# Kernel tuning notes

Measured on AMD Instinct MI355X. Metric: run time of the kernel, lower is better.

## Reference

```python
import jax, jax.numpy as jnp
import numpy as np

N = 50000
NEG_SLOPE = 0.2


def add_self_loops(edge_index, n):
    loop = jnp.arange(n, dtype=edge_index.dtype)
    return jnp.concatenate([edge_index, jnp.stack([loop, loop])], axis=1)


def gatv2_conv(x, edge_index, Wl, bl, Wr, br, att, bias):
    """PyG GATv2Conv (share_weights=False, concat=True, add_self_loops applied by caller).
    x: [N, Fin]; edge_index: [2, E] with row0=src(j), row1=dst(i); att: [H, D].
    Returns (out [N, H*D], alpha [E, H])."""
    src, dst = edge_index[0], edge_index[1]
    H, D = att.shape
    n = x.shape[0]
    xl = (x @ Wl + bl).reshape(n, H, D)   # source-side transform
    xr = (x @ Wr + br).reshape(n, H, D)   # target-side transform
    e = jax.nn.leaky_relu(xl[src] + xr[dst], NEG_SLOPE)        # [E, H, D]
    logit = jnp.einsum('ehd,hd->eh', e, att)                    # [E, H]
    # segment softmax over edges grouped by target node
    lmax = jax.ops.segment_max(logit, dst, num_segments=n)      # [N, H]
    ex = jnp.exp(logit - lmax[dst])
    denom = jax.ops.segment_sum(ex, dst, num_segments=n)
    alpha = ex / denom[dst]                                     # [E, H]
    out = jax.ops.segment_sum(alpha[:, :, None] * xl[src], dst, num_segments=n)  # [N, H, D]
    return out.reshape(n, H * D) + bias, alpha


def setup_inputs() -> dict:
    key = jax.random.key(0)
    ks = jax.random.split(key, 16)
    E = 400000
    x = jax.random.normal(ks[0], (N, 23), dtype=jnp.float32)
    edge_index = jax.random.randint(ks[1], (2, E), 0, N, dtype=jnp.int64)
    H1, D1 = 8, 64
    F1 = H1 * D1  # 512
    s = 0.1
    return {
        'x': x,
        'edge_index': edge_index,
        'Wl1': jax.random.normal(ks[2], (23, F1), dtype=jnp.float32) * s,
        'bl1': jnp.zeros((F1,), jnp.float32),
        'Wr1': jax.random.normal(ks[3], (23, F1), dtype=jnp.float32) * s,
        'br1': jnp.zeros((F1,), jnp.float32),
        'att1': jax.random.normal(ks[4], (H1, D1), dtype=jnp.float32) * s,
        'bias1': jnp.zeros((F1,), jnp.float32),
        'Wl2': jax.random.normal(ks[5], (F1, 1), dtype=jnp.float32) * s,
        'bl2': jnp.zeros((1,), jnp.float32),
        'Wr2': jax.random.normal(ks[6], (F1, 1), dtype=jnp.float32) * s,
        'br2': jnp.zeros((1,), jnp.float32),
        'att2': jax.random.normal(ks[7], (1, 1), dtype=jnp.float32) * s,
        'bias2': jnp.zeros((1,), jnp.float32),
    }


def reference(x, edge_index, Wl1, bl1, Wr1, br1, att1, bias1,
              Wl2, bl2, Wr2, br2, att2, bias2):
    ei = add_self_loops(edge_index, N)
    h, _ = gatv2_conv(x, ei, Wl1, bl1, Wr1, br1, att1, bias1)
    h = jax.nn.relu(h)
    h, alpha = gatv2_conv(h, ei, Wl2, bl2, Wr2, br2, att2, bias2)
    return h, alpha
```

## Files before the change

kernel.cpp:

```cpp
#include <hip/hip_runtime.h>
#include <hip/hip_cooperative_groups.h>
#include <math.h>

namespace cg = cooperative_groups;

#define NN 50000
#define E0 400000
#define EE 450000
#define FF 512
#define G1 2048
#define NPB 25
#define MAXD 64
#define LOG2E 1.44269504f
#define NCU 256

typedef _Float16 h2 __attribute__((ext_vector_type(2)));

__device__ __forceinline__ h2 uas_h2(unsigned u) { union { unsigned u; h2 h; } c; c.u = u; return c.h; }
__device__ __forceinline__ unsigned h2as_u(h2 h) { union { unsigned u; h2 h; } c; c.h = h; return c.u; }
__device__ __forceinline__ unsigned packh(float a, float b) {
    h2 hh = { (_Float16)a, (_Float16)b };
    return h2as_u(hh);
}
__device__ __forceinline__ float leaky(float v) { return fmaxf(v, 0.2f * v); }

template <int CTRL>
__device__ __forceinline__ float dpp_add(float v) {
    int x = __builtin_bit_cast(int, v);
    int y = __builtin_amdgcn_update_dpp(0, x, CTRL, 0xF, 0xF, true);
    return v + __builtin_bit_cast(float, y);
}


__device__ __forceinline__ void phase_scatter(
    int e0, int stride, const int* __restrict__ ei,
    int* __restrict__ cnt, int* __restrict__ src_sl)
{
    for (int e = e0; e < EE; e += stride) {
        int src, dst;
        if (e < E0) { src = ei[e]; dst = ei[E0 + e]; }
        else        { src = e - E0; dst = src; }
        int p = atomicAdd(&cnt[dst], 1);
        if (p < MAXD) src_sl[(size_t)dst * MAXD + p] = src;
    }
}

__device__ __forceinline__ void phase_layer1(
    int l, int wid, int wstep,
    const uint4* __restrict__ xlh, const uint4* __restrict__ xrh,
    const float* __restrict__ att, const float* __restrict__ bias1,
    const float* __restrict__ Wl2, const float* __restrict__ bl2,
    const float* __restrict__ Wr2, const float* __restrict__ br2,
    const int* __restrict__ cnt, const int* __restrict__ src_sl,
    float* __restrict__ xl2, float* __restrict__ xr2)
{
    float4 atA = ((const float4*)att)[2 * l];
    float4 atB = ((const float4*)att)[2 * l + 1];
    h2 a6_0 = { (_Float16)(0.6f * LOG2E * atA.x), (_Float16)(0.6f * LOG2E * atA.y) };
    h2 a6_1 = { (_Float16)(0.6f * LOG2E * atA.z), (_Float16)(0.6f * LOG2E * atA.w) };
    h2 a6_2 = { (_Float16)(0.6f * LOG2E * atB.x), (_Float16)(0.6f * LOG2E * atB.y) };
    h2 a6_3 = { (_Float16)(0.6f * LOG2E * atB.z), (_Float16)(0.6f * LOG2E * atB.w) };
    h2 a4_0 = { (_Float16)(0.4f * LOG2E * atA.x), (_Float16)(0.4f * LOG2E * atA.y) };
    h2 a4_1 = { (_Float16)(0.4f * LOG2E * atA.z), (_Float16)(0.4f * LOG2E * atA.w) };
    h2 a4_2 = { (_Float16)(0.4f * LOG2E * atB.x), (_Float16)(0.4f * LOG2E * atB.y) };
    h2 a4_3 = { (_Float16)(0.4f * LOG2E * atB.z), (_Float16)(0.4f * LOG2E * atB.w) };
    float bl2v = bl2[0], br2v = br2[0];

    int i = wid;
    int dg0 = 0, myj = 0; uint4 xq = {0, 0, 0, 0};
    if (i < NN) {
        dg0 = cnt[i];
        myj = src_sl[(size_t)i * MAXD + l];
        xq  = xrh[(size_t)i * 64 + l];
    }

    for (; i < NN; i += wstep) {
        int dg = dg0; if (dg > MAXD) dg = MAXD;

        int s0 = 0;
        int s1 = (dg > 1) ? 1 : 0;
        int s2 = (dg > 2) ? 2 : s1;
        int s3 = (dg > 3) ? 3 : s2;
        uint4 ra = xlh[(size_t)__builtin_amdgcn_readlane(myj, s0) * 64 + l];
        uint4 rb = xlh[(size_t)__builtin_amdgcn_readlane(myj, s1) * 64 + l];
        uint4 rc = xlh[(size_t)__builtin_amdgcn_readlane(myj, s2) * 64 + l];
        uint4 rd = xlh[(size_t)__builtin_amdgcn_readlane(myj, s3) * 64 + l];

        int inext = i + wstep;
        int dg_n = 0, myj_n = 0; uint4 xq_n = {0, 0, 0, 0};
        if (inext < NN) {
            dg_n  = cnt[inext];
            myj_n = src_sl[(size_t)inext * MAXD + l];
            xq_n  = xrh[(size_t)inext * 64 + l];
        }

        h2 q0 = uas_h2(xq.x), q1 = uas_h2(xq.y), q2 = uas_h2(xq.z), q3 = uas_h2(xq.w);

        float s = 0.f;
        h2 A0 = { 0, 0 }, A1 = { 0, 0 }, A2 = { 0, 0 }, A3 = { 0, 0 };

#define PROC(RV)                                                               \
        {                                                                      \
            h2 p0 = uas_h2(RV.x), p1 = uas_h2(RV.y),                           \
               p2 = uas_h2(RV.z), p3 = uas_h2(RV.w);                           \
            h2 t0 = p0 + q0, t1 = p1 + q1, t2 = p2 + q2, t3 = p3 + q3;         \
            h2 b0 = uas_h2(h2as_u(t0) & 0x7fff7fffu);                          \
            h2 b1 = uas_h2(h2as_u(t1) & 0x7fff7fffu);                          \
            h2 b2 = uas_h2(h2as_u(t2) & 0x7fff7fffu);                          \
            h2 b3 = uas_h2(h2as_u(t3) & 0x7fff7fffu);                          \
            float part = 0.f;                                                  \
            part = __builtin_amdgcn_fdot2(a6_0, t0, part, false);              \
            part = __builtin_amdgcn_fdot2(a4_0, b0, part, false);              \
            part = __builtin_amdgcn_fdot2(a6_1, t1, part, false);              \
            part = __builtin_amdgcn_fdot2(a4_1, b1, part, false);              \
            part = __builtin_amdgcn_fdot2(a6_2, t2, part, false);              \
            part = __builtin_amdgcn_fdot2(a4_2, b2, part, false);              \
            part = __builtin_amdgcn_fdot2(a6_3, t3, part, false);              \
            part = __builtin_amdgcn_fdot2(a4_3, b3, part, false);              \
            part = dpp_add<0xB1>(part);                                        \
            part = dpp_add<0x4E>(part);                                        \
            part = dpp_add<0x141>(part);                                       \
            float wv = exp2f(part);                                            \
            s += wv;                                                           \
            _Float16 wh = (_Float16)wv;                                        \
            h2 w2 = { wh, wh };                                                \
            A0 += w2 * p0;                                                     \
            A1 += w2 * p1;                                                     \
            A2 += w2 * p2;                                                     \
            A3 += w2 * p3;                                                     \
        }

        int p = 0;
        for (;;) {
            PROC(ra);
            if (++p >= dg) break;
            { int sl = p + 3 < dg ? p + 3 : dg - 1;
              ra = xlh[(size_t)__builtin_amdgcn_readlane(myj, sl) * 64 + l]; }
            PROC(rb);
            if (++p >= dg) break;
            { int sl = p + 3 < dg ? p + 3 : dg - 1;
              rb = xlh[(size_t)__builtin_amdgcn_readlane(myj, sl) * 64 + l]; }
            PROC(rc);
            if (++p >= dg) break;
            { int sl = p + 3 < dg ? p + 3 : dg - 1;
              rc = xlh[(size_t)__builtin_amdgcn_readlane(myj, sl) * 64 + l]; }
            PROC(rd);
            if (++p >= dg) break;
            { int sl = p + 3 < dg ? p + 3 : dg - 1;
              rd = xlh[(size_t)__builtin_amdgcn_readlane(myj, sl) * 64 + l]; }
        }
#undef PROC

        float inv = 1.f / s;
        float4 bA = ((const float4*)bias1)[2 * l];
        float4 bB = ((const float4*)bias1)[2 * l + 1];
        float h0 = fmaxf(fmaf((float)A0[0], inv, bA.x), 0.f);
        float h1 = fmaxf(fmaf((float)A0[1], inv, bA.y), 0.f);
        float h2v = fmaxf(fmaf((float)A1[0], inv, bA.z), 0.f);
        float h3 = fmaxf(fmaf((float)A1[1], inv, bA.w), 0.f);
        float h4 = fmaxf(fmaf((float)A2[0], inv, bB.x), 0.f);
        float h5 = fmaxf(fmaf((float)A2[1], inv, bB.y), 0.f);
        float h6 = fmaxf(fmaf((float)A3[0], inv, bB.z), 0.f);
        float h7 = fmaxf(fmaf((float)A3[1], inv, bB.w), 0.f);

        float4 wlA = ((const float4*)Wl2)[2 * l];
        float4 wlB = ((const float4*)Wl2)[2 * l + 1];
        float4 wrA = ((const float4*)Wr2)[2 * l];
        float4 wrB = ((const float4*)Wr2)[2 * l + 1];
        float pl = h0 * wlA.x + h1 * wlA.y + h2v * wlA.z + h3 * wlA.w
                 + h4 * wlB.x + h5 * wlB.y + h6 * wlB.z + h7 * wlB.w;
        float pr = h0 * wrA.x + h1 * wrA.y + h2v * wrA.z + h3 * wrA.w
                 + h4 * wrB.x + h5 * wrB.y + h6 * wrB.z + h7 * wrB.w;
#pragma unroll
        for (int o = 32; o > 0; o >>= 1) {
            pl += __shfl_xor(pl, o, 64);
            pr += __shfl_xor(pr, o, 64);
        }
        if (l == 0) {
            xl2[i] = pl + bl2v;
            xr2[i] = pr + br2v;
        }

        dg0 = dg_n; myj = myj_n; xq = xq_n;
    }
}

__device__ __forceinline__ void phase_l2a(
    int i0, int stride,
    const float* __restrict__ xl2, const float* __restrict__ xr2,
    const float* __restrict__ att2, const float* __restrict__ bias2,
    const int* __restrict__ cnt, const int* __restrict__ src_sl,
    float* __restrict__ out, float* __restrict__ invs)
{
    for (int i = i0; i < NN; i += stride) {
        int dg = cnt[i]; if (dg > MAXD) dg = MAXD;
        const int* sp = src_sl + (size_t)i * MAXD;
        float xri = xr2[i];
        float a2l = att2[0] * LOG2E;
        float s = 0.f, num = 0.f;
        float va = xl2[sp[0]];
        float vb = (1 < dg) ? xl2[sp[1]] : 0.f;
        float vc = (2 < dg) ? xl2[sp[2]] : 0.f;
        float vd = (3 < dg) ? xl2[sp[3]] : 0.f;
        for (int p = 0; p < dg; p++) {
            float v = va; va = vb; vb = vc; vc = vd;
            vd = (p + 4 < dg) ? xl2[sp[p + 4]] : 0.f;
            float w = exp2f(leaky(v + xri) * a2l);
            s += w;
            num = fmaf(w, v, num);
        }
        out[i] = num / s + bias2[0];
        invs[i] = 1.f / s;
    }
}

__device__ __forceinline__ void phase_l2b(
    int e0, int stride,
    const float* __restrict__ xl2, const float* __restrict__ xr2,
    const float* __restrict__ att2, const int* __restrict__ ei,
    const float* __restrict__ invs, float* __restrict__ out)
{
    for (int e = e0; e < EE; e += stride) {
        int src, dst;
        if (e < E0) { src = ei[e]; dst = ei[E0 + e]; }
        else        { src = e - E0; dst = src; }
        float a2l = att2[0] * LOG2E;
        float lg = leaky(xl2[src] + xr2[dst]) * a2l;
        out[NN + e] = exp2f(lg) * invs[dst];
    }
}


__global__ __launch_bounds__(256) void k_pregemm(
    const float* __restrict__ x,
    const float* __restrict__ Wl1, const float* __restrict__ bl1,
    const float* __restrict__ Wr1, const float* __restrict__ br1,
    unsigned* __restrict__ xlh, unsigned* __restrict__ xrh,
    int* __restrict__ cnt)
{
    __shared__ unsigned sxh[NPB * 12];
    int b = blockIdx.x, t = threadIdx.x;

    int z = b * 256 + t;
    if (z < NN) cnt[z] = 0;

    int i0 = b * NPB;
    int i1 = i0 + NPB; if (i1 > NN) i1 = NN;
    int nnod = i1 - i0;
    for (int k = t; k < nnod * 12; k += 256) {
        int n = k / 12, j = k - n * 12;
        const float* row = x + (size_t)(i0 + n) * 23;
        float f0 = row[2 * j];
        float f1 = (2 * j + 1 < 23) ? row[2 * j + 1] : 0.f;
        sxh[n * 12 + j] = packh(f0, f1);
    }

    int c0 = 2 * t, c1 = 2 * t + 1;
    h2 wl0[12], wl1v[12], wr0[12], wr1v[12];
#pragma unroll
    for (int j = 0; j < 12; j++) {
        int r0 = 2 * j, r1 = 2 * j + 1;
        float a, b2;
        a = Wl1[r0 * FF + c0]; b2 = (r1 < 23) ? Wl1[r1 * FF + c0] : 0.f;
        wl0[j] = (h2){ (_Float16)a, (_Float16)b2 };
        a = Wl1[r0 * FF + c1]; b2 = (r1 < 23) ? Wl1[r1 * FF + c1] : 0.f;
        wl1v[j] = (h2){ (_Float16)a, (_Float16)b2 };
        a = Wr1[r0 * FF + c0]; b2 = (r1 < 23) ? Wr1[r1 * FF + c0] : 0.f;
        wr0[j] = (h2){ (_Float16)a, (_Float16)b2 };
        a = Wr1[r0 * FF + c1]; b2 = (r1 < 23) ? Wr1[r1 * FF + c1] : 0.f;
        wr1v[j] = (h2){ (_Float16)a, (_Float16)b2 };
    }
    float bl0 = bl1[c0], bl1s = bl1[c1];
    float br0 = br1[c0], br1s = br1[c1];
    __syncthreads();

    const uint4* S = (const uint4*)sxh;
    uint4 xa = S[0], xb = S[1], xc = S[2];
    for (int n = 0; n < nnod; n++) {
        uint4 na = xa, nb = xb, nc = xc;
        if (n + 1 < nnod) {
            na = S[(n + 1) * 3 + 0];
            nb = S[(n + 1) * 3 + 1];
            nc = S[(n + 1) * 3 + 2];
        }
        h2 xv[12] = { uas_h2(xa.x), uas_h2(xa.y), uas_h2(xa.z), uas_h2(xa.w),
                      uas_h2(xb.x), uas_h2(xb.y), uas_h2(xb.z), uas_h2(xb.w),
                      uas_h2(xc.x), uas_h2(xc.y), uas_h2(xc.z), uas_h2(xc.w) };
        float al0 = bl0, al1 = bl1s, ar0 = br0, ar1 = br1s;
#pragma unroll
        for (int j = 0; j < 12; j++) {
            al0 = __builtin_amdgcn_fdot2(wl0[j], xv[j], al0, false);
            al1 = __builtin_amdgcn_fdot2(wl1v[j], xv[j], al1, false);
            ar0 = __builtin_amdgcn_fdot2(wr0[j], xv[j], ar0, false);
            ar1 = __builtin_amdgcn_fdot2(wr1v[j], xv[j], ar1, false);
        }
        xlh[(size_t)(i0 + n) * 256 + t] = packh(al0, al1);
        xrh[(size_t)(i0 + n) * 256 + t] = packh(ar0, ar1);
        xa = na; xb = nb; xc = nc;
    }
}

__global__ __launch_bounds__(256, 8) void k_fused(
    const uint4* __restrict__ xlh, const uint4* __restrict__ xrh,
    const float* __restrict__ att, const float* __restrict__ bias1,
    const float* __restrict__ Wl2, const float* __restrict__ bl2,
    const float* __restrict__ Wr2, const float* __restrict__ br2,
    int* __restrict__ cnt, int* __restrict__ src_sl,
    float* __restrict__ xl2, float* __restrict__ xr2,
    const int* __restrict__ ei,
    const float* __restrict__ att2, const float* __restrict__ bias2,
    float* __restrict__ out, float* __restrict__ invs)
{
    cg::grid_group grid = cg::this_grid();
    int t = threadIdx.x;
    int gtid = blockIdx.x * 256 + t;
    int stride = gridDim.x * 256;

    phase_scatter(gtid, stride, ei, cnt, src_sl);
    grid.sync();
    phase_layer1(t & 63, blockIdx.x * 4 + (t >> 6), gridDim.x * 4,
                 xlh, xrh, att, bias1, Wl2, bl2, Wr2, br2,
                 cnt, src_sl, xl2, xr2);
    grid.sync();
    phase_l2a(gtid, stride, xl2, xr2, att2, bias2, cnt, src_sl, out, invs);
    grid.sync();
    phase_l2b(gtid, stride, xl2, xr2, att2, ei, invs, out);
}

__global__ __launch_bounds__(256) void k_scatter(
    const int* __restrict__ ei, int* __restrict__ cnt, int* __restrict__ src_sl)
{
    phase_scatter(blockIdx.x * 256 + threadIdx.x, gridDim.x * 256, ei, cnt, src_sl);
}

__global__ __launch_bounds__(256) void k_l1(
    const uint4* __restrict__ xlh, const uint4* __restrict__ xrh,
    const float* __restrict__ att, const float* __restrict__ bias1,
    const float* __restrict__ Wl2, const float* __restrict__ bl2,
    const float* __restrict__ Wr2, const float* __restrict__ br2,
    const int* __restrict__ cnt, const int* __restrict__ src_sl,
    float* __restrict__ xl2, float* __restrict__ xr2)
{
    int t = threadIdx.x;
    phase_layer1(t & 63, blockIdx.x * 4 + (t >> 6), gridDim.x * 4,
                 xlh, xrh, att, bias1, Wl2, bl2, Wr2, br2,
                 cnt, src_sl, xl2, xr2);
}

__global__ __launch_bounds__(256) void k_l2a(
    const float* __restrict__ xl2, const float* __restrict__ xr2,
    const float* __restrict__ att2, const float* __restrict__ bias2,
    const int* __restrict__ cnt, const int* __restrict__ src_sl,
    float* __restrict__ out, float* __restrict__ invs)
{
    phase_l2a(blockIdx.x * 256 + threadIdx.x, gridDim.x * 256,
              xl2, xr2, att2, bias2, cnt, src_sl, out, invs);
}

__global__ __launch_bounds__(256) void k_l2b(
    const float* __restrict__ xl2, const float* __restrict__ xr2,
    const float* __restrict__ att2, const int* __restrict__ ei,
    const float* __restrict__ invs, float* __restrict__ out)
{
    phase_l2b(blockIdx.x * 256 + threadIdx.x, gridDim.x * 256,
              xl2, xr2, att2, ei, invs, out);
}

extern "C" void kernel_launch(void* const* d_in, const int* in_sizes, int n_in,
                              void* d_out, int out_size, void* d_ws, size_t ws_size,
                              hipStream_t stream)
{
    const float* x     = (const float*)d_in[0];
    const int*   ei    = (const int*)d_in[1];
    const float* Wl1   = (const float*)d_in[2];
    const float* bl1   = (const float*)d_in[3];
    const float* Wr1   = (const float*)d_in[4];
    const float* br1   = (const float*)d_in[5];
    const float* att1  = (const float*)d_in[6];
    const float* bias1 = (const float*)d_in[7];
    const float* Wl2   = (const float*)d_in[8];
    const float* bl2   = (const float*)d_in[9];
    const float* Wr2   = (const float*)d_in[10];
    const float* br2   = (const float*)d_in[11];
    const float* att2  = (const float*)d_in[12];
    const float* bias2 = (const float*)d_in[13];
    float* outp = (float*)d_out;

    char* ws = (char*)d_ws;
    unsigned* xlh  = (unsigned*)ws; ws += (size_t)NN * 256 * 4;
    unsigned* xrh  = (unsigned*)ws; ws += (size_t)NN * 256 * 4;
    float* xl2     = (float*)ws;    ws += (size_t)NN * 4;
    float* xr2     = (float*)ws;    ws += (size_t)NN * 4;
    float* invs    = (float*)ws;    ws += (size_t)NN * 4;
    int* cnt       = (int*)ws;      ws += (size_t)NN * 4;
    int* src_sl    = (int*)ws;      ws += (size_t)NN * MAXD * 4;

    k_pregemm<<<G1, 256, 0, stream>>>(x, Wl1, bl1, Wr1, br1, xlh, xrh, cnt);

    static int coopGrid = -1;
    if (coopGrid < 0) {
        int nb = 0;
        if (hipOccupancyMaxActiveBlocksPerMultiprocessor(&nb, k_fused, 256, 0)
                != hipSuccess)
            nb = 0;
        coopGrid = nb * NCU;
        if (coopGrid > G1) coopGrid = G1;
    }

    const uint4* xlh4 = (const uint4*)xlh;
    const uint4* xrh4 = (const uint4*)xrh;

    bool done = false;
    if (coopGrid >= 1536) {
        void* kargs[] = {
            (void*)&xlh4, (void*)&xrh4, (void*)&att1, (void*)&bias1,
            (void*)&Wl2, (void*)&bl2, (void*)&Wr2, (void*)&br2,
            (void*)&cnt, (void*)&src_sl, (void*)&xl2, (void*)&xr2,
            (void*)&ei, (void*)&att2, (void*)&bias2,
            (void*)&outp, (void*)&invs
        };
        if (hipLaunchCooperativeKernel((void*)k_fused, dim3(coopGrid), dim3(256),
                                       kargs, 0, stream) == hipSuccess)
            done = true;
    }
    if (!done) {
        k_scatter<<<(EE + 255) / 256, 256, 0, stream>>>(ei, cnt, src_sl);
        k_l1<<<G1, 256, 0, stream>>>(xlh4, xrh4, att1, bias1, Wl2, bl2, Wr2, br2,
                                     cnt, src_sl, xl2, xr2);
        k_l2a<<<(NN + 255) / 256, 256, 0, stream>>>(xl2, xr2, att2, bias2,
                                                    cnt, src_sl, outp, invs);
        k_l2b<<<(EE + 255) / 256, 256, 0, stream>>>(xl2, xr2, att2, ei, invs, outp);
    }
}
```

Measured before the change: 228.3 us.

## Fold edge scatter into pregemm and replace cooperative launch with atomic barrier

The edge-to-destination scatter moves into the pregemm kernel, which now handles 220 edges per block alongside its node GEMM, so one grid sync phase goes away. The cooperative launch and cg grid.sync are replaced by a normal launch of a persistent kernel that syncs through a hand-written atomic grid barrier, and cnt and the barrier words are zeroed by a memset. This targets cooperative-launch overhead and the cost of cg grid syncs. In exchange it relies on every block of a normal launch being co-resident, which nothing guarantees, and it drops the (256,8) launch bound, which may change occupancy and so the grid size.

```diff
diff --git a/kernel.cpp b/kernel.cpp
--- a/kernel.cpp
+++ b/kernel.cpp
@@ -1,8 +1,5 @@
 #include <hip/hip_runtime.h>
-#include <hip/hip_cooperative_groups.h>
 #include <math.h>
-
-namespace cg = cooperative_groups;
 
 #define NN 50000
 #define E0 400000
@@ -10,6 +7,7 @@
 #define FF 512
 #define G1 2048
 #define NPB 25
+#define EPB 220
 #define MAXD 64
 #define LOG2E 1.44269504f
 #define NCU 256
@@ -31,19 +29,24 @@
     return v + __builtin_bit_cast(float, y);
 }
 
-
-__device__ __forceinline__ void phase_scatter(
-    int e0, int stride, const int* __restrict__ ei,
-    int* __restrict__ cnt, int* __restrict__ src_sl)
-{
-    for (int e = e0; e < EE; e += stride) {
-        int src, dst;
-        if (e < E0) { src = ei[e]; dst = ei[E0 + e]; }
-        else        { src = e - E0; dst = src; }
-        int p = atomicAdd(&cnt[dst], 1);
-        if (p < MAXD) src_sl[(size_t)dst * MAXD + p] = src;
-    }
-}
+__device__ __forceinline__ void gridbar(int* bar) {
+    __syncthreads();
+    if (threadIdx.x == 0) {
+        __threadfence();
+        int g = __hip_atomic_load(&bar[1], __ATOMIC_RELAXED, __HIP_MEMORY_SCOPE_AGENT);
+        int a = __hip_atomic_fetch_add(&bar[0], 1, __ATOMIC_ACQ_REL, __HIP_MEMORY_SCOPE_AGENT);
+        if (a == (int)gridDim.x - 1) {
+            __hip_atomic_store(&bar[0], 0, __ATOMIC_RELAXED, __HIP_MEMORY_SCOPE_AGENT);
+            __hip_atomic_fetch_add(&bar[1], 1, __ATOMIC_RELEASE, __HIP_MEMORY_SCOPE_AGENT);
+        } else {
+            while (__hip_atomic_load(&bar[1], __ATOMIC_ACQUIRE, __HIP_MEMORY_SCOPE_AGENT) == g)
+                __builtin_amdgcn_s_sleep(2);
+        }
+        __threadfence();
+    }
+    __syncthreads();
+}
+
 
 __device__ __forceinline__ void phase_layer1(
     int l, int wid, int wstep,
@@ -231,18 +234,25 @@
 }
 
 
-__global__ __launch_bounds__(256) void k_pregemm(
+__global__ __launch_bounds__(256) void k_predeg(
     const float* __restrict__ x,
     const float* __restrict__ Wl1, const float* __restrict__ bl1,
     const float* __restrict__ Wr1, const float* __restrict__ br1,
+    const int* __restrict__ ei,
     unsigned* __restrict__ xlh, unsigned* __restrict__ xrh,
-    int* __restrict__ cnt)
+    int* __restrict__ cnt, int* __restrict__ src_sl)
 {
     __shared__ unsigned sxh[NPB * 12];
     int b = blockIdx.x, t = threadIdx.x;
 
-    int z = b * 256 + t;
-    if (z < NN) cnt[z] = 0;
+    int e0 = b * EPB;
+    int e1 = e0 + EPB; if (e1 > EE) e1 = EE;
+    int e = e0 + t;
+    int esrc = 0, edst = -1;
+    if (e < e1) {
+        if (e < E0) { esrc = ei[e]; edst = ei[E0 + e]; }
+        else        { esrc = e - E0; edst = esrc; }
+    }
 
     int i0 = b * NPB;
     int i1 = i0 + NPB; if (i1 > NN) i1 = NN;
@@ -298,39 +308,35 @@
         xrh[(size_t)(i0 + n) * 256 + t] = packh(ar0, ar1);
         xa = na; xb = nb; xc = nc;
     }
-}
-
-__global__ __launch_bounds__(256, 8) void k_fused(
+
+    if (edst >= 0) {
+        int p = atomicAdd(&cnt[edst], 1);
+        if (p < MAXD) src_sl[(size_t)edst * MAXD + p] = esrc;
+    }
+}
+
+__global__ __launch_bounds__(256) void k_persist(
     const uint4* __restrict__ xlh, const uint4* __restrict__ xrh,
     const float* __restrict__ att, const float* __restrict__ bias1,
     const float* __restrict__ Wl2, const float* __restrict__ bl2,
     const float* __restrict__ Wr2, const float* __restrict__ br2,
-    int* __restrict__ cnt, int* __restrict__ src_sl,
+    const int* __restrict__ cnt, const int* __restrict__ src_sl,
     float* __restrict__ xl2, float* __restrict__ xr2,
     const int* __restrict__ ei,
     const float* __restrict__ att2, const float* __restrict__ bias2,
-    float* __restrict__ out, float* __restrict__ invs)
-{
-    cg::grid_group grid = cg::this_grid();
+    float* __restrict__ out, float* __restrict__ invs,
+    int* __restrict__ bar)
+{
     int t = threadIdx.x;
-    int gtid = blockIdx.x * 256 + t;
-    int stride = gridDim.x * 256;
-
-    phase_scatter(gtid, stride, ei, cnt, src_sl);
-    grid.sync();
     phase_layer1(t & 63, blockIdx.x * 4 + (t >> 6), gridDim.x * 4,
                  xlh, xrh, att, bias1, Wl2, bl2, Wr2, br2,
                  cnt, src_sl, xl2, xr2);
-    grid.sync();
-    phase_l2a(gtid, stride, xl2, xr2, att2, bias2, cnt, src_sl, out, invs);
-    grid.sync();
-    phase_l2b(gtid, stride, xl2, xr2, att2, ei, invs, out);
-}
-
-__global__ __launch_bounds__(256) void k_scatter(
-    const int* __restrict__ ei, int* __restrict__ cnt, int* __restrict__ src_sl)
-{
-    phase_scatter(blockIdx.x * 256 + threadIdx.x, gridDim.x * 256, ei, cnt, src_sl);
+    gridbar(bar);
+    phase_l2a(blockIdx.x * 256 + t, gridDim.x * 256,
+              xl2, xr2, att2, bias2, cnt, src_sl, out, invs);
+    gridbar(bar);
+    phase_l2b(blockIdx.x * 256 + t, gridDim.x * 256,
+              xl2, xr2, att2, ei, invs, out);
 }
 
 __global__ __launch_bounds__(256) void k_l1(
@@ -393,38 +399,32 @@
     float* xr2     = (float*)ws;    ws += (size_t)NN * 4;
     float* invs    = (float*)ws;    ws += (size_t)NN * 4;
     int* cnt       = (int*)ws;      ws += (size_t)NN * 4;
+    int* bar       = (int*)ws;      ws += 2 * 4;
     int* src_sl    = (int*)ws;      ws += (size_t)NN * MAXD * 4;
 
-    k_pregemm<<<G1, 256, 0, stream>>>(x, Wl1, bl1, Wr1, br1, xlh, xrh, cnt);
-
-    static int coopGrid = -1;
-    if (coopGrid < 0) {
+    (void)hipMemsetAsync(cnt, 0, (size_t)NN * 4 + 8, stream);
+
+    k_predeg<<<G1, 256, 0, stream>>>(x, Wl1, bl1, Wr1, br1, ei, xlh, xrh,
+                                     cnt, src_sl);
+
+    static int persGrid = -1;
+    if (persGrid < 0) {
         int nb = 0;
-        if (hipOccupancyMaxActiveBlocksPerMultiprocessor(&nb, k_fused, 256, 0)
+        if (hipOccupancyMaxActiveBlocksPerMultiprocessor(&nb, k_persist, 256, 0)
                 != hipSuccess)
             nb = 0;
-        coopGrid = nb * NCU;
-        if (coopGrid > G1) coopGrid = G1;
+        persGrid = nb * NCU;
+        if (persGrid > G1) persGrid = G1;
     }
 
     const uint4* xlh4 = (const uint4*)xlh;
     const uint4* xrh4 = (const uint4*)xrh;
 
-    bool done = false;
-    if (coopGrid >= 1536) {
-        void* kargs[] = {
-            (void*)&xlh4, (void*)&xrh4, (void*)&att1, (void*)&bias1,
-            (void*)&Wl2, (void*)&bl2, (void*)&Wr2, (void*)&br2,
-            (void*)&cnt, (void*)&src_sl, (void*)&xl2, (void*)&xr2,
-            (void*)&ei, (void*)&att2, (void*)&bias2,
-            (void*)&outp, (void*)&invs
-        };
-        if (hipLaunchCooperativeKernel((void*)k_fused, dim3(coopGrid), dim3(256),
-                                       kargs, 0, stream) == hipSuccess)
-            done = true;
-    }
-    if (!done) {
-        k_scatter<<<(EE + 255) / 256, 256, 0, stream>>>(ei, cnt, src_sl);
+    if (persGrid >= 4 * NCU) {
+        k_persist<<<persGrid, 256, 0, stream>>>(
+            xlh4, xrh4, att1, bias1, Wl2, bl2, Wr2, br2,
+            cnt, src_sl, xl2, xr2, ei, att2, bias2, outp, invs, bar);
+    } else {
         k_l1<<<G1, 256, 0, stream>>>(xlh4, xrh4, att1, bias1, Wl2, bl2, Wr2, br2,
                                      cnt, src_sl, xl2, xr2);
         k_l2a<<<(NN + 255) / 256, 256, 0, stream>>>(xl2, xr2, att2, bias2,
```

Result: faster. 215.3 us (-5.7%).
